# Kernel tuning notes

Hardware: AMD Instinct MI355X
Metric: run time of the kernel (lower is better)

The kernel has to match this reference:

```python
import jax, jax.numpy as jnp
import numpy as np
import math

N = 20000      # nodes
E = 150000     # edges
IN = 256       # in_dim
HID = 256      # n_hid / out_dim
T = 4          # num_types
R = 8          # num_relations
H = 8          # n_heads
DK = HID // H  # d_k = 32
L = 2          # n_layers
MAXLEN = 240   # RTE max_len


def _rte_table():
    # fixed sinusoid table from RelTemporalEncoding (requires_grad=False in torch)
    pos = np.arange(MAXLEN, dtype=np.float64)[:, None]
    div = np.exp(np.arange(0, HID, 2, dtype=np.float64) * -(math.log(10000.0) / HID))
    emb = np.zeros((MAXLEN, HID), dtype=np.float64)
    emb[:, 0::2] = np.sin(pos * div) / math.sqrt(HID)
    emb[:, 1::2] = np.cos(pos * div) / math.sqrt(HID)
    return jnp.asarray(emb, dtype=jnp.float32)


def setup_inputs() -> dict:
    key = jax.random.key(0)
    ks = jax.random.split(key, 20)
    node_feature = jax.random.normal(ks[0], (N, IN), jnp.float32)
    node_type = jax.random.randint(ks[1], (N,), 0, T)
    edge_index = jax.random.randint(ks[2], (2, E), 0, N)
    edge_type = jax.random.randint(ks[3], (E,), 0, R)
    edge_time = jax.random.randint(ks[4], (E,), 0, MAXLEN)

    s_in = 1.0 / math.sqrt(IN)
    s_h = 1.0 / math.sqrt(HID)
    s_g = math.sqrt(2.0 / (DK + DK))  # glorot for relation mats

    adapt_W = jax.random.normal(ks[5], (T, IN, HID), jnp.float32) * s_in
    adapt_b = jnp.zeros((T, HID), jnp.float32)
    k_W = jax.random.normal(ks[6], (L, T, HID, HID), jnp.float32) * s_h
    k_b = jnp.zeros((L, T, HID), jnp.float32)
    q_W = jax.random.normal(ks[7], (L, T, HID, HID), jnp.float32) * s_h
    q_b = jnp.zeros((L, T, HID), jnp.float32)
    v_W = jax.random.normal(ks[8], (L, T, HID, HID), jnp.float32) * s_h
    v_b = jnp.zeros((L, T, HID), jnp.float32)
    a_W = jax.random.normal(ks[9], (L, T, HID, HID), jnp.float32) * s_h
    a_b = jnp.zeros((L, T, HID), jnp.float32)
    rel_pri = jnp.ones((L, R, H), jnp.float32)
    rel_att = jax.random.normal(ks[10], (L, R, H, DK, DK), jnp.float32) * s_g
    rel_msg = jax.random.normal(ks[11], (L, R, H, DK, DK), jnp.float32) * s_g
    skip = jnp.ones((L, T), jnp.float32)
    rte_W = jax.random.normal(ks[12], (L, HID, HID), jnp.float32) * s_h
    rte_b = jnp.zeros((L, HID), jnp.float32)
    rte_emb = _rte_table()

    return dict(node_feature=node_feature, node_type=node_type, edge_time=edge_time,
                edge_index=edge_index, edge_type=edge_type,
                adapt_W=adapt_W, adapt_b=adapt_b, k_W=k_W, k_b=k_b, q_W=q_W, q_b=q_b,
                v_W=v_W, v_b=v_b, a_W=a_W, a_b=a_b, rel_pri=rel_pri, rel_att=rel_att,
                rel_msg=rel_msg, skip=skip, rte_W=rte_W, rte_b=rte_b, rte_emb=rte_emb)


def _typed_linear(x, W, b, types):
    # x: [M, din]; W: [T, din, dout]; per-row type-selected linear (T dense GEMMs + select)
    out = jnp.zeros((x.shape[0], W.shape[-1]), x.dtype)
    for t in range(T):
        out = jnp.where((types == t)[:, None], x @ W[t] + b[t], out)
    return out


def _hgt_forward(node_feature, node_type, edge_time, edge_index, edge_type,
                 adapt_W, adapt_b, k_W, k_b, q_W, q_b, v_W, v_b, a_W, a_b,
                 rel_pri, rel_att, rel_msg, skip, rte_W, rte_b, rte_emb):
    # adapt: per-type tanh(Linear) (dropout is identity at p=0)
    x = jnp.tanh(_typed_linear(node_feature, adapt_W, adapt_b, node_type))
    src, tgt = edge_index[0], edge_index[1]   # j (source), i (target)
    st, tt = node_type[src], node_type[tgt]
    sqrt_dk = math.sqrt(DK)
    att = None
    rte = rte_emb[edge_time]                  # [E, HID]
    for l in range(L):
        x_j = x[src] + (rte @ rte_W[l] + rte_b[l])   # RTE added to source repr
        x_i = x[tgt]
        q = _typed_linear(x_i, q_W[l], q_b[l], tt).reshape(E, H, DK)
        k = _typed_linear(x_j, k_W[l], k_b[l], st).reshape(E, H, DK)
        v = _typed_linear(x_j, v_W[l], v_b[l], st).reshape(E, H, DK)
        att_e = jnp.zeros((E, H), x.dtype)
        msg = jnp.zeros((E, H, DK), x.dtype)
        for r in range(R):
            kr = jnp.einsum('ehd,hdk->ehk', k, rel_att[l, r])
            vr = jnp.einsum('ehd,hdk->ehk', v, rel_msg[l, r])
            a = (q * kr).sum(-1) * rel_pri[l, r] / sqrt_dk
            m = edge_type == r
            att_e = jnp.where(m[:, None], a, att_e)
            msg = jnp.where(m[:, None, None], vr, msg)
        # segment softmax over target node ids
        amax = jax.ops.segment_max(att_e, tgt, num_segments=N)
        ex = jnp.exp(att_e - amax[tgt])
        denom = jax.ops.segment_sum(ex, tgt, num_segments=N)
        alpha = ex / denom[tgt]                       # [E, H]
        agg = jax.ops.segment_sum(msg * alpha[:, :, None], tgt, num_segments=N)
        agg = jax.nn.gelu(agg.reshape(N, HID), approximate=False)
        trans = _typed_linear(agg, a_W[l], a_b[l], node_type)
        sk = jax.nn.sigmoid(skip[l])[node_type][:, None]
        x = trans * sk + x * (1.0 - sk)               # no LayerNorm (use_norm=False)
        att = alpha
    return att, x


def reference(node_feature, node_type, edge_time, edge_index, edge_type,
              adapt_W, adapt_b, k_W, k_b, q_W, q_b, v_W, v_b, a_W, a_b,
              rel_pri, rel_att, rel_msg, skip, rte_W, rte_b, rte_emb):
    return _hgt_forward(node_feature, node_type, edge_time, edge_index, edge_type,
                        adapt_W, adapt_b, k_W, k_b, q_W, q_b, v_W, v_b, a_W, a_b,
                        rel_pri, rel_att, rel_msg, skip, rte_W, rte_b, rte_emb)
```

## Files before the change

### kernel.cpp

```cpp
#include <hip/hip_runtime.h>
#include <hip/hip_fp16.h>

#define NN    20000
#define NE    150000
#define HD    256
#define NT    4
#define NR    8
#define NH    8
#define DKq   32
#define NL    2
#define MAXL  240
#define HBLK  256
#define SCB   ((NN + 255)/256)
#define TMAX  632
#define FOLDN 79
#define FOLDC 15
#define INV_SQRT_DK 0.17677669529663687f

typedef _Float16 f16x4 __attribute__((ext_vector_type(4)));
typedef float    f32x4v __attribute__((ext_vector_type(4)));

__global__ __launch_bounds__(256) void k_nhist(const int* __restrict__ ntype, int* __restrict__ nhist)
{
    __shared__ int h[NT];
    const int tid = threadIdx.x, b = blockIdx.x;
    if (tid < NT) h[tid] = 0;
    __syncthreads();
    const int cn = (NN + HBLK-1)/HBLK;
    const int nEnd = min((b+1)*cn, NN);
    for (int i = b*cn + tid; i < nEnd; i += 256) atomicAdd(&h[ntype[i]], 1);
    __syncthreads();
    if (tid < NT) nhist[b*NT + tid] = h[tid];
}
__global__ void k_nscan(const int* __restrict__ nhist, int* __restrict__ noff, int* __restrict__ nbase,
                        int* __restrict__ tlist, int* __restrict__ tcount)
{
    __shared__ int tot[NT];
    const int tid = threadIdx.x;
    if (tid < NT){
        int s = 0;
        for (int b = 0; b < HBLK; b++) s += nhist[b*NT + tid];
        tot[tid] = s;
    }
    __syncthreads();
    if (tid == 0){ noff[0]=0; for (int t=0;t<NT;t++) noff[t+1]=noff[t]+tot[t]; }
    if (tid < NT){
        int base = 0; for (int t=0;t<tid;t++) base += tot[t];
        int run = 0;
        for (int b=0;b<HBLK;b++){ nbase[b*NT+tid] = base + run; run += nhist[b*NT+tid]; }
    }
    __syncthreads();
    if (tid == 0){
        int c = 0;
        for (int t = 0; t < NT; t++){
            const int ntile = (tot[t] + 31) >> 5;
            for (int rt = 0; rt < ntile; rt++) tlist[c++] = (t << 20) | rt;
        }
        *tcount = c;
    }
}
__global__ __launch_bounds__(256) void k_nscatter(const int* __restrict__ ntype,
    const int* __restrict__ nbase, int* __restrict__ nbucket)
{
    __shared__ int cur[NT];
    const int tid = threadIdx.x, b = blockIdx.x;
    if (tid < NT) cur[tid] = nbase[b*NT + tid];
    __syncthreads();
    const int cn = (NN + HBLK-1)/HBLK;
    const int nEnd = min((b+1)*cn, NN);
    for (int i = b*cn + tid; i < nEnd; i += 256)
        nbucket[atomicAdd(&cur[ntype[i]], 1)] = i;
}

__global__ void k_zero_bins(int* __restrict__ cnt){
    int i = blockIdx.x*256 + threadIdx.x;
    if (i < NN) cnt[i] = 0;
}
__global__ void k_csr_hist(const int* __restrict__ ei, int* __restrict__ cnt){
    int e = blockIdx.x*256 + threadIdx.x;
    if (e >= NE) return;
    atomicAdd(&cnt[ei[NE+e]], 1);
}
__global__ __launch_bounds__(256) void k_scan1(const int* __restrict__ cnt,
    int* __restrict__ tgt_off, int* __restrict__ bsum)
{
    __shared__ int sh[256];
    const int t = threadIdx.x, b = blockIdx.x;
    const int i = b*256 + t;
    const int v = (i < NN) ? cnt[i] : 0;
    sh[t] = v;
    __syncthreads();
    #pragma unroll
    for (int d = 1; d < 256; d <<= 1){
        const int u = (t >= d) ? sh[t-d] : 0;
        __syncthreads();
        sh[t] += u;
        __syncthreads();
    }
    if (i < NN) tgt_off[i] = sh[t] - v;
    if (t == 255) bsum[b] = sh[255];
}
__global__ __launch_bounds__(128) void k_scan2(const int* __restrict__ bsum,
    int* __restrict__ bbase, int* __restrict__ tgt_off)
{
    __shared__ int sh[128];
    const int t = threadIdx.x;
    const int v = (t < SCB) ? bsum[t] : 0;
    sh[t] = v;
    __syncthreads();
    #pragma unroll
    for (int d = 1; d < 128; d <<= 1){
        const int u = (t >= d) ? sh[t-d] : 0;
        __syncthreads();
        sh[t] += u;
        __syncthreads();
    }
    if (t < SCB) bbase[t] = sh[t] - v;
    if (t == 0) tgt_off[NN] = NE;
}
__global__ __launch_bounds__(256) void k_scan3(int* __restrict__ tgt_off,
    const int* __restrict__ bbase, int* __restrict__ binCur)
{
    const int i = blockIdx.x*256 + threadIdx.x;
    if (i >= NN) return;
    const int o = tgt_off[i] + bbase[blockIdx.x];
    tgt_off[i] = o;
    binCur[i] = o;
}
__global__ void k_csr_scatter(const int* __restrict__ ei, const int* __restrict__ etype,
    const int* __restrict__ etime, const int* __restrict__ ntype,
    int* __restrict__ binCur, int* __restrict__ src_s, int* __restrict__ combo_s,
    int* __restrict__ eid_s)
{
    int e = blockIdx.x*256 + threadIdx.x;
    if (e >= NE) return;
    const int tgt = ei[NE+e], r = etype[e], src = ei[e];
    const int pos = atomicAdd(&binCur[tgt], 1);
    src_s[pos] = src;
    combo_s[pos] = (etime[e]*NT + ntype[src]) | (r << 12);
    eid_s[pos] = e;
}

__global__ __launch_bounds__(256) void k_w2f16_big(
    const float* __restrict__ adaptW, const float* __restrict__ qW, const float* __restrict__ kW,
    const float* __restrict__ vW, const float* __restrict__ aW, _Float16* __restrict__ out)
{
    const int y = blockIdx.y;
    const float* src; int m;
    if (y < 4){ src = adaptW; m = y; }
    else if (y < 12){ src = qW; m = y-4; }
    else if (y < 20){ src = kW; m = y-12; }
    else if (y < 28){ src = vW; m = y-20; }
    else { src = aW; m = y-28; }
    const float* ip = src + (size_t)m*65536;
    _Float16* op = out + (size_t)y*65536;
    const int tid4 = blockIdx.x*256 + threadIdx.x;
    const int k4 = tid4 >> 8, c = tid4 & 255;
    f16x4 hv;
    #pragma unroll
    for (int j = 0; j < 4; j++)
        hv[j] = (_Float16)ip[(size_t)(((k4*4 + j) << 8) + c)];
    *reinterpret_cast<f16x4*>(&op[(size_t)tid4 * 4]) = hv;
}
__global__ __launch_bounds__(256) void k_w2f16_rel(
    const float* __restrict__ attW, const float* __restrict__ msgW, _Float16* __restrict__ out)
{
    const int y = blockIdx.y;
    const float* ip = (y < 128) ? (attW + (size_t)y*1024) : (msgW + (size_t)(y-128)*1024);
    _Float16* op = out + (size_t)y*1024;
    const int tid4 = threadIdx.x;
    const int k4 = tid4 >> 5, c = tid4 & 31;
    f16x4 hv;
    #pragma unroll
    for (int j = 0; j < 4; j++)
        hv[j] = (_Float16)ip[(size_t)(((k4*4 + j) << 5) + c)];
    *reinterpret_cast<f16x4*>(&op[(size_t)tid4 * 4]) = hv;
}

__global__ __launch_bounds__(256) void k_x(
    const float* __restrict__ inF, const _Float16* __restrict__ inH,
    const _Float16* __restrict__ Wb, const float* __restrict__ bb, void* __restrict__ out,
    const int* __restrict__ nbucket, const int* __restrict__ noff,
    const int* __restrict__ tlist, const int* __restrict__ tcount,
    int mode, int oh, const float* __restrict__ skipv, const _Float16* __restrict__ xoldH)
{
    if ((int)blockIdx.x >= *tcount) return;
    const int ent = tlist[blockIdx.x];
    const int t = ent >> 20, rowTile = ent & 0xFFFFF;
    const int start = noff[t], cnt = noff[t+1] - start;

    const int tid = threadIdx.x;
    const int w = tid >> 6, lane = tid & 63;
    const int lrow = lane & 15, lgrp = lane >> 4;

    __shared__ _Float16 Al[32][260];
    __shared__ int nid[32];

    if (tid < 32){
        const int gr = rowTile*32 + tid;
        nid[tid] = (gr < cnt) ? nbucket[start + gr] : -1;
    }
    __syncthreads();
    {
        const int r = tid >> 3;
        const int arow = nid[r];
        if (inH){
            const _Float16* ap = (arow >= 0) ? (inH + (size_t)arow*HD) : nullptr;
            #pragma unroll
            for (int j = 0; j < 8; j++){
                const int f4 = (tid & 7) + j*8;
                f16x4 hv = {0,0,0,0};
                if (ap) hv = *reinterpret_cast<const f16x4*>(ap + f4*4);
                *reinterpret_cast<f16x4*>(&Al[r][f4*4]) = hv;
            }
        } else {
            const float* ap = (arow >= 0) ? (inF + (size_t)arow*HD) : nullptr;
            #pragma unroll
            for (int j = 0; j < 8; j++){
                const int f4 = (tid & 7) + j*8;
                float4 v = make_float4(0.f,0.f,0.f,0.f);
                if (ap) v = *reinterpret_cast<const float4*>(ap + f4*4);
                f16x4 hv;
                hv[0]=(_Float16)v.x; hv[1]=(_Float16)v.y; hv[2]=(_Float16)v.z; hv[3]=(_Float16)v.w;
                *reinterpret_cast<f16x4*>(&Al[r][f4*4]) = hv;
            }
        }
    }
    __syncthreads();

    float sk = 0.f;
    if (mode == 2) sk = 1.f/(1.f + __expf(-skipv[t]));

    const _Float16* W = Wb + (size_t)t*HD*HD;
    const float* bias = bb + (size_t)t*HD;
    f32x4v acc[4][2];
    #pragma unroll
    for (int cs = 0; cs < 4; cs++){
        acc[cs][0] = (f32x4v){0.f,0.f,0.f,0.f};
        acc[cs][1] = (f32x4v){0.f,0.f,0.f,0.f};
    }
    #pragma unroll 4
    for (int kc = 0; kc < 16; kc++){
        f16x4 bf[4];
        #pragma unroll
        for (int cs = 0; cs < 4; cs++)
            bf[cs] = *reinterpret_cast<const f16x4*>(
                &W[(size_t)((kc*4 + lgrp)*HD + w*64 + cs*16 + lrow)*4]);
        const f16x4 af0 = *reinterpret_cast<const f16x4*>(&Al[lrow][kc*16 + lgrp*4]);
        const f16x4 af1 = *reinterpret_cast<const f16x4*>(&Al[16 + lrow][kc*16 + lgrp*4]);
        #pragma unroll
        for (int cs = 0; cs < 4; cs++){
            acc[cs][0] = __builtin_amdgcn_mfma_f32_16x16x16f16(af0, bf[cs], acc[cs][0], 0,0,0);
            acc[cs][1] = __builtin_amdgcn_mfma_f32_16x16x16f16(af1, bf[cs], acc[cs][1], 0,0,0);
        }
    }
    #pragma unroll
    for (int cs = 0; cs < 4; cs++){
        const int col = w*64 + cs*16 + lrow;
        const float bcol = bias[col];
        #pragma unroll
        for (int rt = 0; rt < 2; rt++){
            #pragma unroll
            for (int i = 0; i < 4; i++){
                const int lr = rt*16 + lgrp*4 + i;
                const int gr = rowTile*32 + lr;
                if (gr >= cnt) continue;
                const int node = nid[lr];
                float v = acc[cs][rt][i] + bcol;
                if (mode == 1) v = tanhf(v);
                else if (mode == 2){
                    const float xo = (float)xoldH[(size_t)node*HD + col];
                    v = v*sk + xo*(1.f - sk);
                }
                if (oh) ((_Float16*)out)[(size_t)node*HD + col] = (_Float16)v;
                else    ((float*)out)[(size_t)node*HD + col] = v;
            }
        }
    }
}

__global__ __launch_bounds__(256) void k_qkv(
    const _Float16* __restrict__ xh,
    const _Float16* __restrict__ Wq, const float* __restrict__ bq, _Float16* __restrict__ oq,
    const _Float16* __restrict__ Wk, const float* __restrict__ bk, _Float16* __restrict__ okk,
    const _Float16* __restrict__ Wv, const float* __restrict__ bv, _Float16* __restrict__ ov,
    const int* __restrict__ nbucket, const int* __restrict__ noff,
    const int* __restrict__ tlist, const int* __restrict__ tcount)
{
    if ((int)blockIdx.x >= *tcount) return;
    const int ent = tlist[blockIdx.x];
    const int t = ent >> 20, rowTile = ent & 0xFFFFF;
    const int start = noff[t], cnt = noff[t+1] - start;
    const int sel = blockIdx.y;
    const _Float16* Wb = (sel==0 ? Wq : (sel==1 ? Wk : Wv));
    const float* bb = (sel==0 ? bq : (sel==1 ? bk : bv));
    _Float16* out = (sel==0 ? oq : (sel==1 ? okk : ov));

    const int tid = threadIdx.x;
    const int w = tid >> 6, lane = tid & 63;
    const int lrow = lane & 15, lgrp = lane >> 4;

    __shared__ _Float16 Al[32][260];
    __shared__ int nid[32];

    if (tid < 32){
        const int gr = rowTile*32 + tid;
        nid[tid] = (gr < cnt) ? nbucket[start + gr] : -1;
    }
    __syncthreads();
    {
        const int r = tid >> 3;
        const int arow = nid[r];
        const _Float16* ap = (arow >= 0) ? (xh + (size_t)arow*HD) : nullptr;
        #pragma unroll
        for (int j = 0; j < 8; j++){
            const int f4 = (tid & 7) + j*8;
            f16x4 hv = {0,0,0,0};
            if (ap) hv = *reinterpret_cast<const f16x4*>(ap + f4*4);
            *reinterpret_cast<f16x4*>(&Al[r][f4*4]) = hv;
        }
    }
    __syncthreads();

    const _Float16* W = Wb + (size_t)t*HD*HD;
    const float* bias = bb + (size_t)t*HD;
    f32x4v acc[4][2];
    #pragma unroll
    for (int cs = 0; cs < 4; cs++){
        acc[cs][0] = (f32x4v){0.f,0.f,0.f,0.f};
        acc[cs][1] = (f32x4v){0.f,0.f,0.f,0.f};
    }
    #pragma unroll 4
    for (int kc = 0; kc < 16; kc++){
        f16x4 bf[4];
        #pragma unroll
        for (int cs = 0; cs < 4; cs++)
            bf[cs] = *reinterpret_cast<const f16x4*>(
                &W[(size_t)((kc*4 + lgrp)*HD + w*64 + cs*16 + lrow)*4]);
        const f16x4 af0 = *reinterpret_cast<const f16x4*>(&Al[lrow][kc*16 + lgrp*4]);
        const f16x4 af1 = *reinterpret_cast<const f16x4*>(&Al[16 + lrow][kc*16 + lgrp*4]);
        #pragma unroll
        for (int cs = 0; cs < 4; cs++){
            acc[cs][0] = __builtin_amdgcn_mfma_f32_16x16x16f16(af0, bf[cs], acc[cs][0], 0,0,0);
            acc[cs][1] = __builtin_amdgcn_mfma_f32_16x16x16f16(af1, bf[cs], acc[cs][1], 0,0,0);
        }
    }
    #pragma unroll
    for (int cs = 0; cs < 4; cs++){
        const int col = w*64 + cs*16 + lrow;
        const float bcol = bias[col];
        #pragma unroll
        for (int rt = 0; rt < 2; rt++){
            #pragma unroll
            for (int i = 0; i < 4; i++){
                const int lr = rt*16 + lgrp*4 + i;
                const int gr = rowTile*32 + lr;
                if (gr >= cnt) continue;
                const int node = nid[lr];
                out[(size_t)node*HD + col] = (_Float16)(acc[cs][rt][i] + bcol);
            }
        }
    }
}

__global__ __launch_bounds__(256) void k_row_gemm(
    const float* __restrict__ A, const float* __restrict__ W, const float* __restrict__ bias,
    float* __restrict__ C)
{
    const int row = blockIdx.x, d = threadIdx.x;
    __shared__ float ar[HD];
    ar[d] = A[(size_t)row*HD + d];
    __syncthreads();
    float acc = bias[d];
    #pragma unroll 8
    for (int k=0;k<HD;k++) acc = fmaf(ar[k], W[(size_t)k*HD + d], acc);
    C[(size_t)row*HD + d] = acc;
}
__global__ __launch_bounds__(256) void k_row_gemm2(
    const float* __restrict__ A, const float* __restrict__ kWb, const float* __restrict__ vWb,
    _Float16* __restrict__ Kc, _Float16* __restrict__ Vc)
{
    const int row = blockIdx.x, ty = blockIdx.y, d = threadIdx.x;
    const float* W = ((blockIdx.z == 0) ? kWb : vWb) + (size_t)ty*HD*HD;
    _Float16* C = (blockIdx.z == 0) ? Kc : Vc;
    __shared__ float ar[HD];
    ar[d] = A[(size_t)row*HD + d];
    __syncthreads();
    float acc = 0.f;
    #pragma unroll 8
    for (int k=0;k<HD;k++) acc = fmaf(ar[k], W[(size_t)k*HD + d], acc);
    C[(size_t)row*(NT*HD) + ty*HD + d] = (_Float16)acc;
}

__global__ __launch_bounds__(256) void k_fold_mfma(
    const _Float16* __restrict__ IN, const _Float16* __restrict__ MATF,
    _Float16* __restrict__ OUT, int M, int nbx)
{
    const int r = blockIdx.y;
    const int lane = threadIdx.x & 63, w = threadIdx.x >> 6;
    const int lrow = lane & 15, lgrp = lane >> 4;
    f16x4 b[NH][2][2];
    const _Float16* Mr = MATF + (size_t)r*NH*1024;
    #pragma unroll
    for (int h = 0; h < NH; h++)
      #pragma unroll
      for (int kb = 0; kb < 2; kb++)
        #pragma unroll
        for (int hf = 0; hf < 2; hf++)
            b[h][kb][hf] = *reinterpret_cast<const f16x4*>(
                &Mr[(size_t)h*1024 + (size_t)(((kb*4 + lgrp)*32) + hf*16 + lrow)*4]);
    const int ntiles = M >> 4;
    for (int t = (int)blockIdx.x*4 + w; t < ntiles; t += nbx*4){
        const int row0 = t*16;
        const _Float16* inrow = IN + (size_t)(row0 + lrow)*HD;
        f16x4 a[NH][2];
        #pragma unroll
        for (int h = 0; h < NH; h++)
          #pragma unroll
          for (int kb = 0; kb < 2; kb++)
              a[h][kb] = *reinterpret_cast<const f16x4*>(&inrow[h*32 + kb*16 + lgrp*4]);
        #pragma unroll
        for (int h = 0; h < NH; h++){
          #pragma unroll
          for (int hf = 0; hf < 2; hf++){
              f32x4v acc = {0.f,0.f,0.f,0.f};
              acc = __builtin_amdgcn_mfma_f32_16x16x16f16(a[h][0], b[h][0][hf], acc, 0,0,0);
              acc = __builtin_amdgcn_mfma_f32_16x16x16f16(a[h][1], b[h][1][hf], acc, 0,0,0);
              #pragma unroll
              for (int i = 0; i < 4; i++){
                  const int rr = lgrp*4 + i;
                  OUT[((size_t)(row0+rr)*NR + r)*HD + h*32 + hf*16 + lrow] = (_Float16)acc[i];
              }
          }
        }
    }
}

__global__ __launch_bounds__(256) void k_scoresm(
    const _Float16* __restrict__ q0, const _Float16* __restrict__ kA, const _Float16* __restrict__ KcA,
    const float* __restrict__ relP,
    const int* __restrict__ tgt_off, const int* __restrict__ src_s, const int* __restrict__ combo_s,
    float* __restrict__ s_arr, float* __restrict__ mbuf, float* __restrict__ lbuf)
{
    const int n = blockIdx.x*4 + (threadIdx.x >> 6);
    if (n >= NN) return;
    const int lane = threadIdx.x & 63;
    const int h = lane >> 3, c4 = (lane & 7) << 2;
    const int col = h*32 + c4;
    const int e0 = tgt_off[n], e1 = tgt_off[n+1];
    if (e0 == e1) return;

    const f16x4 qh = *reinterpret_cast<const f16x4*>(&q0[(size_t)n*HD + col]);
    const float q0v = (float)qh[0], q1v = (float)qh[1], q2v = (float)qh[2], q3v = (float)qh[3];
    float m = -INFINITY, l = 0.f;
    for (int j = e0; j < e1; j++){
        const int src = src_s[j];
        const int cw  = combo_s[j];
        const int r = cw >> 12, combo = cw & 0xFFF;
        const f16x4 ka = *reinterpret_cast<const f16x4*>(&kA[((size_t)src*NR + r)*HD + col]);
        const f16x4 kc = *reinterpret_cast<const f16x4*>(&KcA[((size_t)combo*NR + r)*HD + col]);
        float s = q0v*((float)ka[0]+(float)kc[0])
                + q1v*((float)ka[1]+(float)kc[1])
                + q2v*((float)ka[2]+(float)kc[2])
                + q3v*((float)ka[3]+(float)kc[3]);
        s += __shfl_xor(s, 1); s += __shfl_xor(s, 2); s += __shfl_xor(s, 4);
        s *= relP[r*NH + h] * INV_SQRT_DK;
        if ((lane & 7) == 0) s_arr[(size_t)j*NH + h] = s;
        const float mn = fmaxf(m, s);
        l = l*__expf(m - mn) + __expf(s - mn);
        m = mn;
    }
    if ((lane & 7) == 0){
        mbuf[(size_t)n*NH + h] = m;
        lbuf[(size_t)n*NH + h] = l;
    }
}

__global__ __launch_bounds__(256) void k_agg(
    const _Float16* __restrict__ vM, const _Float16* __restrict__ VcM,
    const float* __restrict__ s_arr, const float* __restrict__ mbuf, const float* __restrict__ lbuf,
    const int* __restrict__ tgt_off, const int* __restrict__ src_s, const int* __restrict__ combo_s,
    const int* __restrict__ eid_s,
    _Float16* __restrict__ agg, float* __restrict__ out_att, int store_s)
{
    const int n = blockIdx.x*4 + (threadIdx.x >> 6);
    if (n >= NN) return;
    const int lane = threadIdx.x & 63;
    const int h = lane >> 3, c4 = (lane & 7) << 2;
    const int col = h*32 + c4;
    const int e0 = tgt_off[n], e1 = tgt_off[n+1];

    float m = 0.f, inv = 0.f;
    if (e0 < e1){
        m = mbuf[(size_t)n*NH + h];
        inv = 1.f / lbuf[(size_t)n*NH + h];
    }
    float a0=0.f, a1=0.f, a2=0.f, a3=0.f;
    for (int j = e0; j < e1; j++){
        const int src = src_s[j];
        const int cw  = combo_s[j];
        const int r = cw >> 12, combo = cw & 0xFFF;
        const float al = __expf(s_arr[(size_t)j*NH + h] - m) * inv;
        const f16x4 vm = *reinterpret_cast<const f16x4*>(&vM[((size_t)src*NR + r)*HD + col]);
        const f16x4 vc = *reinterpret_cast<const f16x4*>(&VcM[((size_t)combo*NR + r)*HD + col]);
        a0 = fmaf(al, (float)vm[0] + (float)vc[0], a0);
        a1 = fmaf(al, (float)vm[1] + (float)vc[1], a1);
        a2 = fmaf(al, (float)vm[2] + (float)vc[2], a2);
        a3 = fmaf(al, (float)vm[3] + (float)vc[3], a3);
        if (store_s && (lane & 7) == 0) out_att[(size_t)eid_s[j]*NH + h] = al;
    }
    f16x4 o;
    o[0] = (_Float16)(0.5f*a0*(1.f + erff(a0*0.70710678118654752f)));
    o[1] = (_Float16)(0.5f*a1*(1.f + erff(a1*0.70710678118654752f)));
    o[2] = (_Float16)(0.5f*a2*(1.f + erff(a2*0.70710678118654752f)));
    o[3] = (_Float16)(0.5f*a3*(1.f + erff(a3*0.70710678118654752f)));
    *reinterpret_cast<f16x4*>(&agg[(size_t)n*HD + col]) = o;
}

extern "C" void kernel_launch(void* const* d_in, const int* in_sizes, int n_in,
                              void* d_out, int out_size, void* d_ws, size_t ws_size,
                              hipStream_t stream)
{
    const float* node_feature = (const float*)d_in[0];
    const int*   node_type    = (const int*)d_in[1];
    const int*   edge_time    = (const int*)d_in[2];
    const int*   edge_index   = (const int*)d_in[3];
    const int*   edge_type    = (const int*)d_in[4];
    const float* adapt_W = (const float*)d_in[5];
    const float* adapt_b = (const float*)d_in[6];
    const float* k_W = (const float*)d_in[7];
    const float* k_b = (const float*)d_in[8];
    const float* q_W = (const float*)d_in[9];
    const float* q_b = (const float*)d_in[10];
    const float* v_W = (const float*)d_in[11];
    const float* v_b = (const float*)d_in[12];
    const float* a_W = (const float*)d_in[13];
    const float* a_b = (const float*)d_in[14];
    const float* rel_pri = (const float*)d_in[15];
    const float* rel_att = (const float*)d_in[16];
    const float* rel_msg = (const float*)d_in[17];
    const float* skip  = (const float*)d_in[18];
    const float* rte_W = (const float*)d_in[19];
    const float* rte_b = (const float*)d_in[20];
    const float* rte_emb = (const float*)d_in[21];

    char* wp = (char*)d_ws;
    auto alloc_f = [&](size_t n)->float*{ float* p=(float*)wp; wp += n*sizeof(float); return p; };
    auto alloc_i = [&](size_t n)->int*  { int*   p=(int*)wp;   wp += n*sizeof(int);   return p; };
    auto alloc_h = [&](size_t n)->_Float16*{ _Float16* p=(_Float16*)wp; wp += n*sizeof(_Float16); return p; };
    _Float16* xh0 = alloc_h((size_t)NN*HD);
    _Float16* xh1 = alloc_h((size_t)NN*HD);
    _Float16* q0h = alloc_h((size_t)NN*HD);
    _Float16* k0h = alloc_h((size_t)NN*HD);
    _Float16* v0h = alloc_h((size_t)NN*HD);
    _Float16* aggh= alloc_h((size_t)NN*HD);
    float* s_arr = alloc_f((size_t)NE*NH);
    float* mbuf  = alloc_f((size_t)NN*NH);
    float* lbuf  = alloc_f((size_t)NN*NH);
    float* rteP  = alloc_f((size_t)MAXL*HD);
    _Float16* Kch = alloc_h((size_t)MAXL*NT*HD);
    _Float16* Vch = alloc_h((size_t)MAXL*NT*HD);
    _Float16* kavm = alloc_h((size_t)NN*NR*HD);
    _Float16* kcaA0 = alloc_h((size_t)MAXL*NT*NR*HD);
    _Float16* kcaA1 = alloc_h((size_t)MAXL*NT*NR*HD);
    _Float16* kcaM0 = alloc_h((size_t)MAXL*NT*NR*HD);
    _Float16* kcaM1 = alloc_h((size_t)MAXL*NT*NR*HD);
    _Float16* wF   = alloc_h((size_t)36*65536);
    _Float16* relF = alloc_h((size_t)256*1024);
    int* nbucket = alloc_i(NN);
    int* nhist   = alloc_i(HBLK*NT);
    int* nbase   = alloc_i(HBLK*NT);
    int* noff    = alloc_i(8);
    int* tlist   = alloc_i(TMAX);
    int* tcount  = alloc_i(8);
    int* cnt     = alloc_i(NN);
    int* bsum    = alloc_i(SCB);
    int* bbase   = alloc_i(SCB);
    int* binCur  = alloc_i(NN);
    int* tgt_off = alloc_i(NN+1);
    int* src_s   = alloc_i(NE);
    int* combo_s = alloc_i(NE);
    int* eid_s   = alloc_i(NE);

    const _Float16* adaptF = wF;
    const _Float16* qF = wF + (size_t)4*65536;
    const _Float16* kF = wF + (size_t)12*65536;
    const _Float16* vF = wF + (size_t)20*65536;
    const _Float16* aF = wF + (size_t)28*65536;
    const _Float16* relAF = relF;
    const _Float16* relMF = relF + (size_t)128*1024;

    float* out_att = (float*)d_out;
    float* out_x   = (float*)d_out + (size_t)NE*NH;

    const dim3 gFoldN(FOLDN, NR);
    const dim3 gFoldC(FOLDC, NR);
    const dim3 gQKV(TMAX, 3);
    const int gE256 = (NE + 255)/256;
    const int gEg = (NN + 3)/4;

    k_w2f16_big<<<dim3(64,36),256,0,stream>>>(adapt_W, q_W, k_W, v_W, a_W, wF);
    k_w2f16_rel<<<dim3(1,256),256,0,stream>>>(rel_att, rel_msg, relF);

    k_nhist<<<HBLK,256,0,stream>>>(node_type, nhist);
    k_nscan<<<1,64,0,stream>>>(nhist, noff, nbase, tlist, tcount);
    k_nscatter<<<HBLK,256,0,stream>>>(node_type, nbase, nbucket);

    k_zero_bins<<<SCB,256,0,stream>>>(cnt);
    k_csr_hist<<<gE256,256,0,stream>>>(edge_index, cnt);
    k_scan1<<<SCB,256,0,stream>>>(cnt, tgt_off, bsum);
    k_scan2<<<1,128,0,stream>>>(bsum, bbase, tgt_off);
    k_scan3<<<SCB,256,0,stream>>>(tgt_off, bbase, binCur);
    k_csr_scatter<<<gE256,256,0,stream>>>(edge_index, edge_type, edge_time, node_type,
                                          binCur, src_s, combo_s, eid_s);

    {
        k_row_gemm<<<MAXL,256,0,stream>>>(rte_emb, rte_W, rte_b, rteP);
        k_row_gemm2<<<dim3(MAXL,NT,2),256,0,stream>>>(rteP, k_W, v_W, Kch, Vch);
        k_fold_mfma<<<gFoldC,256,0,stream>>>(Kch, relAF, kcaA0, MAXL*NT, FOLDC);
        k_fold_mfma<<<gFoldC,256,0,stream>>>(Vch, relMF, kcaM0, MAXL*NT, FOLDC);
        k_row_gemm<<<MAXL,256,0,stream>>>(rte_emb, rte_W + (size_t)HD*HD, rte_b + HD, rteP);
        k_row_gemm2<<<dim3(MAXL,NT,2),256,0,stream>>>(rteP, k_W + (size_t)NT*HD*HD,
                                                      v_W + (size_t)NT*HD*HD, Kch, Vch);
        k_fold_mfma<<<gFoldC,256,0,stream>>>(Kch, relAF + (size_t)NR*NH*1024, kcaA1, MAXL*NT, FOLDC);
        k_fold_mfma<<<gFoldC,256,0,stream>>>(Vch, relMF + (size_t)NR*NH*1024, kcaM1, MAXL*NT, FOLDC);
    }

    k_x<<<TMAX,256,0,stream>>>(node_feature, nullptr, adaptF, adapt_b, xh0,
                               nbucket, noff, tlist, tcount, 1, 1, nullptr, nullptr);
    k_qkv<<<gQKV,256,0,stream>>>(xh0, qF, q_b, q0h, kF, k_b, k0h, vF, v_b, v0h,
                                 nbucket, noff, tlist, tcount);

    for (int l = 0; l < NL; l++){
        const _Float16* rAF = relAF + (size_t)l*NR*NH*1024;
        const _Float16* rMF = relMF + (size_t)l*NR*NH*1024;
        const _Float16* kcaA = (l == 0) ? kcaA0 : kcaA1;
        const _Float16* kcaM = (l == 0) ? kcaM0 : kcaM1;
        const int store_s = (l == NL-1) ? 1 : 0;
        k_fold_mfma<<<gFoldN,256,0,stream>>>(k0h, rAF, kavm, NN, FOLDN);
        k_scoresm<<<gEg,256,0,stream>>>(q0h, kavm, kcaA, rel_pri + (size_t)l*NR*NH,
                                        tgt_off, src_s, combo_s, s_arr, mbuf, lbuf);
        k_fold_mfma<<<gFoldN,256,0,stream>>>(v0h, rMF, kavm, NN, FOLDN);
        k_agg<<<gEg,256,0,stream>>>(kavm, kcaM, s_arr, mbuf, lbuf,
                                    tgt_off, src_s, combo_s, eid_s,
                                    aggh, out_att, store_s);
        if (l == 0){
            k_x<<<TMAX,256,0,stream>>>(nullptr, aggh, aF, a_b, xh1,
                                       nbucket, noff, tlist, tcount, 2, 1, skip, xh0);
            k_qkv<<<gQKV,256,0,stream>>>(xh1, qF + (size_t)NT*HD*HD, q_b + (size_t)NT*HD, q0h,
                                         kF + (size_t)NT*HD*HD, k_b + (size_t)NT*HD, k0h,
                                         vF + (size_t)NT*HD*HD, v_b + (size_t)NT*HD, v0h,
                                         nbucket, noff, tlist, tcount);
        } else {
            k_x<<<TMAX,256,0,stream>>>(nullptr, aggh, aF + (size_t)NT*HD*HD, a_b + (size_t)NT*HD,
                                       out_x, nbucket, noff, tlist, tcount, 2, 0, skip + NT, xh1);
        }
    }
}
```

Baseline: 578.3 us.

## Fuse score and aggregation into one online-softmax edge pass; batch K/V folds

Merges the separate score/softmax and aggregation kernels into a single per-target pass that uses an online softmax and rescales the running value accumulator. Each edge's K and V gathers are now issued in the same loop, and attention is written only in the last layer by a separate elementwise kernel that uses a new edge-to-target map. The K and V relation folds are launched together via a z-dimension, which needs a second NN×NR×HD fp16 buffer. This removes one pass over the edges per layer, plus the s_arr round trip in layer 0. In exchange it adds per-edge rescaling arithmetic and extra memory.

```diff
diff --git a/kernel.cpp b/kernel.cpp
--- a/kernel.cpp
+++ b/kernel.cpp
@@ -139,6 +139,13 @@
     src_s[pos] = src;
     combo_s[pos] = (etime[e]*NT + ntype[src]) | (r << 12);
     eid_s[pos] = e;
+}
+__global__ void k_tgtmap(const int* __restrict__ tgt_off, int* __restrict__ tgt_srt)
+{
+    const int n = blockIdx.x*256 + threadIdx.x;
+    if (n >= NN) return;
+    const int e0 = tgt_off[n], e1 = tgt_off[n+1];
+    for (int j = e0; j < e1; j++) tgt_srt[j] = n;
 }
 
 __global__ __launch_bounds__(256) void k_w2f16_big(
@@ -392,11 +399,15 @@
     C[(size_t)row*(NT*HD) + ty*HD + d] = (_Float16)acc;
 }
 
-__global__ __launch_bounds__(256) void k_fold_mfma(
-    const _Float16* __restrict__ IN, const _Float16* __restrict__ MATF,
-    _Float16* __restrict__ OUT, int M, int nbx)
+__global__ __launch_bounds__(256) void k_fold2(
+    const _Float16* __restrict__ INa, const _Float16* __restrict__ MATa, _Float16* __restrict__ OUTa,
+    const _Float16* __restrict__ INb, const _Float16* __restrict__ MATb, _Float16* __restrict__ OUTb,
+    int M, int nbx)
 {
     const int r = blockIdx.y;
+    const _Float16* IN = blockIdx.z ? INb : INa;
+    const _Float16* MATF = blockIdx.z ? MATb : MATa;
+    _Float16* OUT = blockIdx.z ? OUTb : OUTa;
     const int lane = threadIdx.x & 63, w = threadIdx.x >> 6;
     const int lrow = lane & 15, lgrp = lane >> 4;
     f16x4 b[NH][2][2];
@@ -436,11 +447,13 @@
     }
 }
 
-__global__ __launch_bounds__(256) void k_scoresm(
+__global__ __launch_bounds__(256) void k_edge(
     const _Float16* __restrict__ q0, const _Float16* __restrict__ kA, const _Float16* __restrict__ KcA,
+    const _Float16* __restrict__ vM, const _Float16* __restrict__ VcM,
     const float* __restrict__ relP,
     const int* __restrict__ tgt_off, const int* __restrict__ src_s, const int* __restrict__ combo_s,
-    float* __restrict__ s_arr, float* __restrict__ mbuf, float* __restrict__ lbuf)
+    _Float16* __restrict__ agg,
+    float* __restrict__ s_arr, float* __restrict__ mbuf, float* __restrict__ lbuf, int store_s)
 {
     const int n = blockIdx.x*4 + (threadIdx.x >> 6);
     if (n >= NN) return;
@@ -448,73 +461,63 @@
     const int h = lane >> 3, c4 = (lane & 7) << 2;
     const int col = h*32 + c4;
     const int e0 = tgt_off[n], e1 = tgt_off[n+1];
-    if (e0 == e1) return;
 
     const f16x4 qh = *reinterpret_cast<const f16x4*>(&q0[(size_t)n*HD + col]);
     const float q0v = (float)qh[0], q1v = (float)qh[1], q2v = (float)qh[2], q3v = (float)qh[3];
     float m = -INFINITY, l = 0.f;
+    float a0=0.f, a1=0.f, a2=0.f, a3=0.f;
+
     for (int j = e0; j < e1; j++){
         const int src = src_s[j];
         const int cw  = combo_s[j];
         const int r = cw >> 12, combo = cw & 0xFFF;
-        const f16x4 ka = *reinterpret_cast<const f16x4*>(&kA[((size_t)src*NR + r)*HD + col]);
-        const f16x4 kc = *reinterpret_cast<const f16x4*>(&KcA[((size_t)combo*NR + r)*HD + col]);
+        const size_t offS = ((size_t)src*NR + r)*HD + col;
+        const size_t offC = ((size_t)combo*NR + r)*HD + col;
+        const f16x4 ka = *reinterpret_cast<const f16x4*>(&kA[offS]);
+        const f16x4 kc = *reinterpret_cast<const f16x4*>(&KcA[offC]);
+        const f16x4 vm = *reinterpret_cast<const f16x4*>(&vM[offS]);
+        const f16x4 vc = *reinterpret_cast<const f16x4*>(&VcM[offC]);
         float s = q0v*((float)ka[0]+(float)kc[0])
                 + q1v*((float)ka[1]+(float)kc[1])
                 + q2v*((float)ka[2]+(float)kc[2])
                 + q3v*((float)ka[3]+(float)kc[3]);
         s += __shfl_xor(s, 1); s += __shfl_xor(s, 2); s += __shfl_xor(s, 4);
         s *= relP[r*NH + h] * INV_SQRT_DK;
-        if ((lane & 7) == 0) s_arr[(size_t)j*NH + h] = s;
+        if (store_s && (lane & 7) == 0) s_arr[(size_t)j*NH + h] = s;
         const float mn = fmaxf(m, s);
-        l = l*__expf(m - mn) + __expf(s - mn);
+        const float sc = __expf(m - mn);
+        const float p  = __expf(s - mn);
+        l = l*sc + p;
         m = mn;
-    }
-    if ((lane & 7) == 0){
-        mbuf[(size_t)n*NH + h] = m;
-        lbuf[(size_t)n*NH + h] = l;
-    }
-}
-
-__global__ __launch_bounds__(256) void k_agg(
-    const _Float16* __restrict__ vM, const _Float16* __restrict__ VcM,
-    const float* __restrict__ s_arr, const float* __restrict__ mbuf, const float* __restrict__ lbuf,
-    const int* __restrict__ tgt_off, const int* __restrict__ src_s, const int* __restrict__ combo_s,
-    const int* __restrict__ eid_s,
-    _Float16* __restrict__ agg, float* __restrict__ out_att, int store_s)
-{
-    const int n = blockIdx.x*4 + (threadIdx.x >> 6);
-    if (n >= NN) return;
-    const int lane = threadIdx.x & 63;
-    const int h = lane >> 3, c4 = (lane & 7) << 2;
-    const int col = h*32 + c4;
-    const int e0 = tgt_off[n], e1 = tgt_off[n+1];
-
-    float m = 0.f, inv = 0.f;
-    if (e0 < e1){
-        m = mbuf[(size_t)n*NH + h];
-        inv = 1.f / lbuf[(size_t)n*NH + h];
-    }
-    float a0=0.f, a1=0.f, a2=0.f, a3=0.f;
-    for (int j = e0; j < e1; j++){
-        const int src = src_s[j];
-        const int cw  = combo_s[j];
-        const int r = cw >> 12, combo = cw & 0xFFF;
-        const float al = __expf(s_arr[(size_t)j*NH + h] - m) * inv;
-        const f16x4 vm = *reinterpret_cast<const f16x4*>(&vM[((size_t)src*NR + r)*HD + col]);
-        const f16x4 vc = *reinterpret_cast<const f16x4*>(&VcM[((size_t)combo*NR + r)*HD + col]);
-        a0 = fmaf(al, (float)vm[0] + (float)vc[0], a0);
-        a1 = fmaf(al, (float)vm[1] + (float)vc[1], a1);
-        a2 = fmaf(al, (float)vm[2] + (float)vc[2], a2);
-        a3 = fmaf(al, (float)vm[3] + (float)vc[3], a3);
-        if (store_s && (lane & 7) == 0) out_att[(size_t)eid_s[j]*NH + h] = al;
-    }
+        a0 = a0*sc + p*((float)vm[0] + (float)vc[0]);
+        a1 = a1*sc + p*((float)vm[1] + (float)vc[1]);
+        a2 = a2*sc + p*((float)vm[2] + (float)vc[2]);
+        a3 = a3*sc + p*((float)vm[3] + (float)vc[3]);
+    }
+    const float inv = (l > 0.f) ? 1.f/l : 0.f;
+    a0 *= inv; a1 *= inv; a2 *= inv; a3 *= inv;
     f16x4 o;
     o[0] = (_Float16)(0.5f*a0*(1.f + erff(a0*0.70710678118654752f)));
     o[1] = (_Float16)(0.5f*a1*(1.f + erff(a1*0.70710678118654752f)));
     o[2] = (_Float16)(0.5f*a2*(1.f + erff(a2*0.70710678118654752f)));
     o[3] = (_Float16)(0.5f*a3*(1.f + erff(a3*0.70710678118654752f)));
     *reinterpret_cast<f16x4*>(&agg[(size_t)n*HD + col]) = o;
+    if (store_s && (lane & 7) == 0){
+        mbuf[(size_t)n*NH + h] = m;
+        lbuf[(size_t)n*NH + h] = l;
+    }
+}
+
+__global__ void k_alpha(const float* __restrict__ s_arr, const int* __restrict__ eid_s,
+                        const float* __restrict__ mbuf, const float* __restrict__ lbuf,
+                        const int* __restrict__ tgt_srt, float* __restrict__ out_att)
+{
+    int i = blockIdx.x*256 + threadIdx.x;
+    if (i >= NE*NH) return;
+    const int j = i >> 3, h = i & 7;
+    const int t = tgt_srt[j];
+    const float a = __expf(s_arr[i] - mbuf[(size_t)t*NH + h]) / lbuf[(size_t)t*NH + h];
+    out_att[(size_t)eid_s[j]*NH + h] = a;
 }
 
 extern "C" void kernel_launch(void* const* d_in, const int* in_sizes, int n_in,
@@ -561,6 +564,7 @@
     _Float16* Kch = alloc_h((size_t)MAXL*NT*HD);
     _Float16* Vch = alloc_h((size_t)MAXL*NT*HD);
     _Float16* kavm = alloc_h((size_t)NN*NR*HD);
+    _Float16* vmh  = alloc_h((size_t)NN*NR*HD);
     _Float16* kcaA0 = alloc_h((size_t)MAXL*NT*NR*HD);
     _Float16* kcaA1 = alloc_h((size_t)MAXL*NT*NR*HD);
     _Float16* kcaM0 = alloc_h((size_t)MAXL*NT*NR*HD);
@@ -581,6 +585,7 @@
     int* src_s   = alloc_i(NE);
     int* combo_s = alloc_i(NE);
     int* eid_s   = alloc_i(NE);
+    int* tgt_srt = alloc_i(NE);
 
     const _Float16* adaptF = wF;
     const _Float16* qF = wF + (size_t)4*65536;
@@ -593,10 +598,12 @@
     float* out_att = (float*)d_out;
     float* out_x   = (float*)d_out + (size_t)NE*NH;
 
-    const dim3 gFoldN(FOLDN, NR);
-    const dim3 gFoldC(FOLDC, NR);
+    const dim3 gFoldN2(FOLDN, NR, 2);
+    const dim3 gFoldC2(FOLDC, NR, 2);
     const dim3 gQKV(TMAX, 3);
     const int gE256 = (NE + 255)/256;
+    const int gEH = (NE*NH + 255)/256;
+    const int gN256 = (NN + 255)/256;
     const int gEg = (NN + 3)/4;
 
     k_w2f16_big<<<dim3(64,36),256,0,stream>>>(adapt_W, q_W, k_W, v_W, a_W, wF);
@@ -613,17 +620,17 @@
     k_scan3<<<SCB,256,0,stream>>>(tgt_off, bbase, binCur);
     k_csr_scatter<<<gE256,256,0,stream>>>(edge_index, edge_type, edge_time, node_type,
                                           binCur, src_s, combo_s, eid_s);
+    k_tgtmap<<<gN256,256,0,stream>>>(tgt_off, tgt_srt);
 
     {
         k_row_gemm<<<MAXL,256,0,stream>>>(rte_emb, rte_W, rte_b, rteP);
         k_row_gemm2<<<dim3(MAXL,NT,2),256,0,stream>>>(rteP, k_W, v_W, Kch, Vch);
-        k_fold_mfma<<<gFoldC,256,0,stream>>>(Kch, relAF, kcaA0, MAXL*NT, FOLDC);
-        k_fold_mfma<<<gFoldC,256,0,stream>>>(Vch, relMF, kcaM0, MAXL*NT, FOLDC);
+        k_fold2<<<gFoldC2,256,0,stream>>>(Kch, relAF, kcaA0, Vch, relMF, kcaM0, MAXL*NT, FOLDC);
         k_row_gemm<<<MAXL,256,0,stream>>>(rte_emb, rte_W + (size_t)HD*HD, rte_b + HD, rteP);
         k_row_gemm2<<<dim3(MAXL,NT,2),256,0,stream>>>(rteP, k_W + (size_t)NT*HD*HD,
                                                       v_W + (size_t)NT*HD*HD, Kch, Vch);
-        k_fold_mfma<<<gFoldC,256,0,stream>>>(Kch, relAF + (size_t)NR*NH*1024, kcaA1, MAXL*NT, FOLDC);
-        k_fold_mfma<<<gFoldC,256,0,stream>>>(Vch, relMF + (size_t)NR*NH*1024, kcaM1, MAXL*NT, FOLDC);
+        k_fold2<<<gFoldC2,256,0,stream>>>(Kch, relAF + (size_t)NR*NH*1024, kcaA1,
+                                          Vch, relMF + (size_t)NR*NH*1024, kcaM1, MAXL*NT, FOLDC);
     }
 
     k_x<<<TMAX,256,0,stream>>>(node_feature, nullptr, adaptF, adapt_b, xh0,
@@ -637,13 +644,13 @@
         const _Float16* kcaA = (l == 0) ? kcaA0 : kcaA1;
         const _Float16* kcaM = (l == 0) ? kcaM0 : kcaM1;
         const int store_s = (l == NL-1) ? 1 : 0;
-        k_fold_mfma<<<gFoldN,256,0,stream>>>(k0h, rAF, kavm, NN, FOLDN);
-        k_scoresm<<<gEg,256,0,stream>>>(q0h, kavm, kcaA, rel_pri + (size_t)l*NR*NH,
-                                        tgt_off, src_s, combo_s, s_arr, mbuf, lbuf);
-        k_fold_mfma<<<gFoldN,256,0,stream>>>(v0h, rMF, kavm, NN, FOLDN);
-        k_agg<<<gEg,256,0,stream>>>(kavm, kcaM, s_arr, mbuf, lbuf,
-                                    tgt_off, src_s, combo_s, eid_s,
-                                    aggh, out_att, store_s);
+        k_fold2<<<gFoldN2,256,0,stream>>>(k0h, rAF, kavm, v0h, rMF, vmh, NN, FOLDN);
+        k_edge<<<gEg,256,0,stream>>>(q0h, kavm, kcaA, vmh, kcaM,
+                                     rel_pri + (size_t)l*NR*NH,
+                                     tgt_off, src_s, combo_s, aggh,
+                                     s_arr, mbuf, lbuf, store_s);
+        if (store_s)
+            k_alpha<<<gEH,256,0,stream>>>(s_arr, eid_s, mbuf, lbuf, tgt_srt, out_att);
         if (l == 0){
             k_x<<<TMAX,256,0,stream>>>(nullptr, aggh, aF, a_b, xh1,
                                        nbucket, noff, tlist, tcount, 2, 1, skip, xh0);
```

Result: faster. 539.4 us (median of 2 runs) (-6.7%).
